# Kernel optimization log

Hardware: AMD Instinct MI355X
Metric: run time of the kernel (lower is better)

The kernel has to match this reference:

```python
import jax, jax.numpy as jnp
import numpy as np

D_IN = 768
D_OUT = 768
NUM_HEADS = 12


def setup_inputs() -> dict:
    key = jax.random.key(0)
    kx, kq, kk, kv, ko = jax.random.split(key, 5)
    x = jax.random.normal(kx, (4, 2048, D_IN), dtype=jnp.float32)
    # torch.rand -> uniform [0,1)
    w_query = jax.random.uniform(kq, (D_IN, D_OUT), dtype=jnp.float32)
    w_key = jax.random.uniform(kk, (D_IN, D_OUT), dtype=jnp.float32)
    w_value = jax.random.uniform(kv, (D_IN, D_OUT), dtype=jnp.float32)
    out_proj = jax.random.uniform(ko, (D_IN, D_OUT), dtype=jnp.float32)
    return {"x": x, "w_query": w_query, "w_key": w_key, "w_value": w_value, "out_proj": out_proj}


def reference(x, w_query, w_key, w_value, out_proj):
    b, n, _ = x.shape
    hd = D_OUT // NUM_HEADS  # head_dim
    q = (x @ w_query).reshape(b, n, NUM_HEADS, hd).transpose(0, 2, 1, 3)  # [b,h,n,hd]
    k = (x @ w_key).reshape(b, n, NUM_HEADS, hd).transpose(0, 2, 1, 3)
    v = (x @ w_value).reshape(b, n, NUM_HEADS, hd).transpose(0, 2, 1, 3)
    scores = jnp.einsum('bhqd,bhkd->bhqk', q, k)
    causal = jnp.triu(jnp.ones((n, n), dtype=bool), k=1)
    scores = jnp.where(causal, -jnp.inf, scores)
    attn = jax.nn.softmax(scores / jnp.sqrt(jnp.float32(hd)), axis=-1)
    # dropout p=0.0 -> identity
    ctx = jnp.einsum('bhqk,bhkd->bhqd', attn, v).transpose(0, 2, 1, 3).reshape(b, n, D_OUT)
    return ctx @ out_proj
```

## Files before the change

### kernel.cpp

```cpp
#include <hip/hip_runtime.h>

typedef __bf16    bf16x8 __attribute__((ext_vector_type(8)));
typedef _Float16  f16x8  __attribute__((ext_vector_type(8)));
typedef _Float16  f16x4  __attribute__((ext_vector_type(4)));
typedef float     f32x4  __attribute__((ext_vector_type(4)));

#define MFMA16(a,b,c)  __builtin_amdgcn_mfma_f32_16x16x32_bf16((a),(b),(c),0,0,0)
#define MFMAF16(a,b,c) __builtin_amdgcn_mfma_f32_16x16x32_f16((a),(b),(c),0,0,0)

#define AS1(p) (const __attribute__((address_space(1))) void*)(p)
#define AS3(p) (__attribute__((address_space(3))) void*)(p)
#define GLL16(g, l) __builtin_amdgcn_global_load_lds(AS1(g), AS3(l), 16, 0, 0)

__device__ __forceinline__ float fexp2(float x) {
  float r; asm("v_exp_f32 %0, %1" : "=v"(r) : "v"(x)); return r;
}

#define QSCALE 0.18033688011112042f

__global__ __launch_bounds__(256) void k_conv_x(const float* __restrict__ x,
                                                __bf16* __restrict__ xh,
                                                __bf16* __restrict__ xl) {
  int i = blockIdx.x * 256 + threadIdx.x;
  const float4* p = (const float4*)x + (size_t)i * 2;
  float4 a = p[0], b = p[1];
  float v[8] = {a.x, a.y, a.z, a.w, b.x, b.y, b.z, b.w};
  bf16x8 h, l;
#pragma unroll
  for (int j = 0; j < 8; ++j) {
    __bf16 hh = (__bf16)v[j];
    h[j] = hh;
    l[j] = (__bf16)(v[j] - (float)hh);
  }
  *(bf16x8*)(xh + (size_t)i * 8) = h;
  *(bf16x8*)(xl + (size_t)i * 8) = l;
}

__global__ __launch_bounds__(256) void k_conv_w(const float* __restrict__ wq,
                                                const float* __restrict__ wk,
                                                const float* __restrict__ wv,
                                                const float* __restrict__ op,
                                                __bf16* __restrict__ wt_h,
                                                __bf16* __restrict__ wt_l,
                                                _Float16* __restrict__ wot) {
  __shared__ float tile[32][33];
  int bid = blockIdx.x;
  int m = bid / 576, rem = bid % 576;
  int tr = rem / 24, tc = rem % 24;
  const float* src = (m == 0) ? wq : (m == 1) ? wk : (m == 2) ? wv : op;
  int tx = threadIdx.x & 31, ty = threadIdx.x >> 5;
  int r0 = tr * 32, c0 = tc * 32;
#pragma unroll
  for (int j = 0; j < 4; ++j)
    tile[ty + j * 8][tx] = src[(size_t)(r0 + ty + j * 8) * 768 + c0 + tx];
  __syncthreads();
#pragma unroll
  for (int j = 0; j < 4; ++j) {
    float v = tile[tx][ty + j * 8];
    size_t o = (size_t)(c0 + ty + j * 8) * 768 + r0 + tx;
    if (m < 3) {
      size_t oo = (size_t)m * (768 * 768) + o;
      __bf16 h = (__bf16)v;
      wt_h[oo] = h;
      wt_l[oo] = (__bf16)(v - (float)h);
    } else {
      wot[o] = (_Float16)v;
    }
  }
}

__global__ __launch_bounds__(256) void k_qk_gemm(
    const __bf16* __restrict__ Ah, const __bf16* __restrict__ Al,
    const __bf16* __restrict__ Bh, const __bf16* __restrict__ Bl,
    _Float16* __restrict__ qf_o, _Float16* __restrict__ kf_o) {
  __shared__ __align__(16) __bf16 AsH[2][128 * 32];
  __shared__ __align__(16) __bf16 AsL[2][128 * 32];
  __shared__ __align__(16) __bf16 BsH[2][128 * 32];
  __shared__ __align__(16) __bf16 BsL[2][128 * 32];
  int t = threadIdx.x, lane = t & 63, wid = t >> 6;
  int l15 = lane & 15, lh = lane >> 4;
  int bid = blockIdx.x;
  int mt = bid & 63, nt = bid >> 6;
  int m0 = mt * 128, n0 = nt * 128;
  int wr = wid >> 1, wc = wid & 1;
  f32x4 acc[4][4];
#pragma unroll
  for (int i = 0; i < 4; ++i)
#pragma unroll
    for (int j = 0; j < 4; ++j) acc[i][j] = (f32x4){0.f, 0.f, 0.f, 0.f};

  int row0 = t >> 2;
  int kkA = (((t & 3) ^ ((row0 >> 1) & 3)) << 3);
  char* lAH[2] = {(char*)AsH[0] + wid * 1024, (char*)AsH[1] + wid * 1024};
  char* lAL[2] = {(char*)AsL[0] + wid * 1024, (char*)AsL[1] + wid * 1024};
  char* lBH[2] = {(char*)BsH[0] + wid * 1024, (char*)BsH[1] + wid * 1024};
  char* lBL[2] = {(char*)BsL[0] + wid * 1024, (char*)BsL[1] + wid * 1024};

#define QK_STAGE(bb, k0s) do {                                               \
    size_t a0 = (size_t)(m0 + row0) * 768 + (k0s) + kkA;                     \
    size_t a1 = a0 + (size_t)64 * 768;                                       \
    size_t b0 = (size_t)(n0 + row0) * 768 + (k0s) + kkA;                     \
    size_t b1 = b0 + (size_t)64 * 768;                                       \
    GLL16(Ah + a0, lAH[bb]); GLL16(Ah + a1, lAH[bb] + 4096);                 \
    GLL16(Bh + b0, lBH[bb]); GLL16(Bh + b1, lBH[bb] + 4096);                 \
    GLL16(Al + a0, lAL[bb]); GLL16(Al + a1, lAL[bb] + 4096);                 \
    GLL16(Bl + b0, lBL[bb]); GLL16(Bl + b1, lBL[bb] + 4096);                 \
  } while (0)

  QK_STAGE(0, 0);
  asm volatile("s_waitcnt vmcnt(0)" ::: "memory");
  __syncthreads();

  for (int tt = 0; tt < 24; ++tt) {
    int cur = tt & 1;
    if (tt < 23) QK_STAGE(cur ^ 1, (tt + 1) * 32);

    bf16x8 af[4], alf[4], bf_[4], blf[4];
#pragma unroll
    for (int i = 0; i < 4; ++i) {
      int rowA = wr * 64 + i * 16 + l15;
      int aoff = rowA * 64 + (((lh ^ (rowA >> 1)) & 3) << 4);
      int rowB = wc * 64 + i * 16 + l15;
      int boff = rowB * 64 + (((lh ^ (rowB >> 1)) & 3) << 4);
      af[i]  = *(const bf16x8*)((char*)AsH[cur] + aoff);
      alf[i] = *(const bf16x8*)((char*)AsL[cur] + aoff);
      bf_[i] = *(const bf16x8*)((char*)BsH[cur] + boff);
      blf[i] = *(const bf16x8*)((char*)BsL[cur] + boff);
    }
    __builtin_amdgcn_s_setprio(1);
#pragma unroll
    for (int i = 0; i < 4; ++i)
#pragma unroll
      for (int j = 0; j < 4; ++j) {
        acc[i][j] = MFMA16(af[i], bf_[j], acc[i][j]);
        acc[i][j] = MFMA16(af[i], blf[j], acc[i][j]);
        acc[i][j] = MFMA16(alf[i], bf_[j], acc[i][j]);
      }
    __builtin_amdgcn_s_setprio(0);
    asm volatile("s_waitcnt vmcnt(0)" ::: "memory");
    __syncthreads();
  }
#undef QK_STAGE

#pragma unroll
  for (int j = 0; j < 4; ++j) {
    int c = n0 + wc * 64 + j * 16 + l15;
    int which = c / 768; int cc = c - which * 768;
    int hh = cc >> 6, d = cc & 63;
#pragma unroll
    for (int i = 0; i < 4; ++i)
#pragma unroll
      for (int r = 0; r < 4; ++r) {
        int m = m0 + wr * 64 + i * 16 + lh * 4 + r;
        int bb = m >> 11, n = m & 2047;
        float v = acc[i][j][r];
        size_t o = ((size_t)(bb * 12 + hh) * 2048 + n) * 64 + d;
        if (which == 0) qf_o[o] = (_Float16)(v * QSCALE);
        else            kf_o[o] = (_Float16)v;
      }
  }
}

__global__ __launch_bounds__(256) void k_v_gemm(
    const __bf16* __restrict__ A, const __bf16* __restrict__ Bt,
    _Float16* __restrict__ vT_o) {
  __shared__ __align__(16) __bf16 As[2][128 * 32];
  __shared__ __align__(16) __bf16 Bs[2][128 * 32];
  int t = threadIdx.x, lane = t & 63, wid = t >> 6;
  int l15 = lane & 15, lh = lane >> 4;
  int bid = blockIdx.x;
  int mt = bid & 63, nt = bid >> 6;
  int m0 = mt * 128, n0 = 1536 + nt * 128;
  int wr = wid >> 1, wc = wid & 1;
  f32x4 acc[4][4];
#pragma unroll
  for (int i = 0; i < 4; ++i)
#pragma unroll
    for (int j = 0; j < 4; ++j) acc[i][j] = (f32x4){0.f, 0.f, 0.f, 0.f};
  int row0 = t >> 2;
  int kkA = (((t & 3) ^ ((row0 >> 1) & 3)) << 3);
  char* lA[2] = {(char*)As[0] + wid * 1024, (char*)As[1] + wid * 1024};
  char* lB[2] = {(char*)Bs[0] + wid * 1024, (char*)Bs[1] + wid * 1024};

#define V_STAGE(bb, k0s) do {                                                \
    size_t a0 = (size_t)(m0 + row0) * 768 + (k0s) + kkA;                     \
    size_t b0 = (size_t)(n0 + row0) * 768 + (k0s) + kkA;                     \
    GLL16(A + a0, lA[bb]);  GLL16(A + a0 + (size_t)64 * 768, lA[bb] + 4096); \
    GLL16(Bt + b0, lB[bb]); GLL16(Bt + b0 + (size_t)64 * 768, lB[bb] + 4096);\
  } while (0)

  V_STAGE(0, 0);
  asm volatile("s_waitcnt vmcnt(0)" ::: "memory");
  __syncthreads();

  for (int tt = 0; tt < 24; ++tt) {
    int cur = tt & 1;
    if (tt < 23) V_STAGE(cur ^ 1, (tt + 1) * 32);
    bf16x8 af[4], bf_[4];
#pragma unroll
    for (int i = 0; i < 4; ++i) {
      int rowA = wr * 64 + i * 16 + l15;
      int aoff = rowA * 64 + (((lh ^ (rowA >> 1)) & 3) << 4);
      int rowB = wc * 64 + i * 16 + l15;
      int boff = rowB * 64 + (((lh ^ (rowB >> 1)) & 3) << 4);
      af[i]  = *(const bf16x8*)((char*)As[cur] + aoff);
      bf_[i] = *(const bf16x8*)((char*)Bs[cur] + boff);
    }
    __builtin_amdgcn_s_setprio(1);
#pragma unroll
    for (int i = 0; i < 4; ++i)
#pragma unroll
      for (int j = 0; j < 4; ++j) acc[i][j] = MFMA16(af[i], bf_[j], acc[i][j]);
    __builtin_amdgcn_s_setprio(0);
    asm volatile("s_waitcnt vmcnt(0)" ::: "memory");
    __syncthreads();
  }
#undef V_STAGE

#pragma unroll
  for (int j = 0; j < 4; ++j) {
    int c = n0 + wc * 64 + j * 16 + l15;
    int cc = c - 1536;
    int hh = cc >> 6, d = cc & 63;
#pragma unroll
    for (int i = 0; i < 4; ++i)
#pragma unroll
      for (int r = 0; r < 4; ++r) {
        int m = m0 + wr * 64 + i * 16 + lh * 4 + r;
        int bb = m >> 11, n = m & 2047;
        vT_o[((size_t)(bb * 12 + hh) * 64 + d) * 2048 + n] = (_Float16)acc[i][j][r];
      }
  }
}

__global__ __launch_bounds__(256) void k_attn(
    const _Float16* __restrict__ Qf, const _Float16* __restrict__ Kf,
    const _Float16* __restrict__ Vt, _Float16* __restrict__ ctx) {
  __shared__ __align__(16) _Float16 Ks[2][64 * 64];
  __shared__ __align__(16) _Float16 Vs[2][64 * 64];
  __shared__ __align__(16) _Float16 Pt[4][32 * 64];
  int t = threadIdx.x, lane = t & 63, wid = t >> 6;
  int l15 = lane & 15, lh = lane >> 4;
  int bid = blockIdx.x;
  int bh = bid % 48;
  int qt = 15 - bid / 48;
  int qbase = qt * 128 + wid * 32;
  size_t base = (size_t)bh * (2048 * 64);
  char* ptw = (char*)Pt[wid];

  int skey = t >> 3, sdb = t & 7;
  int ssw = (sdb ^ (skey & 7)) * 8;
  const _Float16* ksrc = Kf + base + (size_t)skey * 64 + ssw;
  const _Float16* vsrc = Vt + base + (size_t)skey * 2048 + ssw;
  char* dK[2] = {(char*)Ks[0] + wid * 1024, (char*)Ks[1] + wid * 1024};
  char* dV[2] = {(char*)Vs[0] + wid * 1024, (char*)Vs[1] + wid * 1024};

#define ATT_STAGE(bb, k0s) do {                                    \
    GLL16(ksrc + (size_t)(k0s) * 64, dK[bb]);                      \
    GLL16(ksrc + (size_t)(k0s) * 64 + 2048, dK[bb] + 4096);        \
    GLL16(vsrc + (k0s), dV[bb]);                                   \
    GLL16(vsrc + (k0s) + 32 * 2048, dV[bb] + 4096);                \
  } while (0)

  f16x8 qf[2][2];
#pragma unroll
  for (int i = 0; i < 2; ++i)
#pragma unroll
    for (int kk = 0; kk < 2; ++kk)
      qf[i][kk] = *(const f16x8*)(Qf + base +
          (size_t)(qbase + i * 16 + l15) * 64 + kk * 32 + lh * 8);

  f32x4 o[2][4];
#pragma unroll
  for (int i = 0; i < 2; ++i)
#pragma unroll
    for (int d = 0; d < 4; ++d) o[i][d] = (f32x4){0.f, 0.f, 0.f, 0.f};
  float mrun[2] = {-1e30f, -1e30f}, lrun[2] = {0.f, 0.f};

  int nIter = 2 * qt + 2;
  ATT_STAGE(0, 0);
  asm volatile("s_waitcnt vmcnt(0)" ::: "memory");
  __syncthreads();

  for (int it = 0; it < nIter; ++it) {
    int cur = it & 1;
    int k0 = it * 64;
    if (it + 1 < nIter) ATT_STAGE(cur ^ 1, k0 + 64);

    if (k0 <= qbase + 31) {
      f32x4 s[4][2];
#pragma unroll
      for (int j = 0; j < 4; ++j)
#pragma unroll
        for (int i = 0; i < 2; ++i) s[j][i] = (f32x4){0.f, 0.f, 0.f, 0.f};
      __builtin_amdgcn_s_setprio(1);
#pragma unroll
      for (int j = 0; j < 4; ++j) {
        int kr = j * 16 + l15;
#pragma unroll
        for (int kk = 0; kk < 2; ++kk) {
          int sw = ((kk * 4 + lh) ^ (kr & 7)) << 4;
          f16x8 kf = *(const f16x8*)((char*)Ks[cur] + kr * 128 + sw);
          s[j][0] = MFMAF16(kf, qf[0][kk], s[j][0]);
          s[j][1] = MFMAF16(kf, qf[1][kk], s[j][1]);
        }
      }
      __builtin_amdgcn_s_setprio(0);

      if (k0 + 63 > qbase) {
#pragma unroll
        for (int j = 0; j < 4; ++j)
#pragma unroll
          for (int i = 0; i < 2; ++i)
#pragma unroll
            for (int r = 0; r < 4; ++r) {
              int key = k0 + j * 16 + lh * 4 + r;
              int qg = qbase + i * 16 + l15;
              if (key > qg) s[j][i][r] = -1e30f;
            }
      }

#pragma unroll
      for (int i = 0; i < 2; ++i) {
        float m01 = fmaxf(fmaxf(s[0][i][0], s[0][i][1]), fmaxf(s[0][i][2], s[0][i][3]));
        float m23 = fmaxf(fmaxf(s[1][i][0], s[1][i][1]), fmaxf(s[1][i][2], s[1][i][3]));
        float m45 = fmaxf(fmaxf(s[2][i][0], s[2][i][1]), fmaxf(s[2][i][2], s[2][i][3]));
        float m67 = fmaxf(fmaxf(s[3][i][0], s[3][i][1]), fmaxf(s[3][i][2], s[3][i][3]));
        float mx = fmaxf(fmaxf(m01, m23), fmaxf(m45, m67));
        mx = fmaxf(mx, __shfl_xor(mx, 16));
        mx = fmaxf(mx, __shfl_xor(mx, 32));
        float mn = fmaxf(mrun[i], mx);
        float alpha = fexp2(mrun[i] - mn);
        mrun[i] = mn;
        float rsum = 0.f;
#pragma unroll
        for (int j = 0; j < 4; ++j)
#pragma unroll
          for (int r = 0; r < 4; ++r) {
            float e = fexp2(s[j][i][r] - mn);
            s[j][i][r] = e;
            rsum += e;
          }
        rsum += __shfl_xor(rsum, 16);
        rsum += __shfl_xor(rsum, 32);
        lrun[i] = lrun[i] * alpha + rsum;
#pragma unroll
        for (int d = 0; d < 4; ++d) o[i][d] *= alpha;
#pragma unroll
        for (int j = 0; j < 4; ++j) {
          f16x4 pk = { (_Float16)s[j][i][0], (_Float16)s[j][i][1],
                       (_Float16)s[j][i][2], (_Float16)s[j][i][3] };
          int row = 16 * i + l15;
          int boff = (row * 128 + j * 32 + lh * 8) ^ ((l15 & 7) << 4);
          *(f16x4*)(ptw + boff) = pk;
        }
      }
      asm volatile("" ::: "memory");
      f16x8 pa[2][2];
#pragma unroll
      for (int i = 0; i < 2; ++i)
#pragma unroll
        for (int kk = 0; kk < 2; ++kk) {
          int row = 16 * i + l15;
          int boff = (row * 128 + kk * 64 + lh * 16) ^ ((l15 & 7) << 4);
          pa[i][kk] = *(const f16x8*)(ptw + boff);
        }
      asm volatile("" ::: "memory");

      __builtin_amdgcn_s_setprio(1);
#pragma unroll
      for (int dt = 0; dt < 4; ++dt) {
        int dr = dt * 16 + l15;
#pragma unroll
        for (int kk = 0; kk < 2; ++kk) {
          int sw = ((kk * 4 + lh) ^ (dr & 7)) << 4;
          f16x8 vf = *(const f16x8*)((char*)Vs[cur] + dr * 128 + sw);
          o[0][dt] = MFMAF16(vf, pa[0][kk], o[0][dt]);
          o[1][dt] = MFMAF16(vf, pa[1][kk], o[1][dt]);
        }
      }
      __builtin_amdgcn_s_setprio(0);
    }
    asm volatile("s_waitcnt vmcnt(0)" ::: "memory");
    __syncthreads();
  }
#undef ATT_STAGE

  int b = bh / 12, hh = bh - (bh / 12) * 12;
  float inv[2] = {1.f / lrun[0], 1.f / lrun[1]};
#pragma unroll
  for (int i = 0; i < 2; ++i)
#pragma unroll
    for (int dt = 0; dt < 4; ++dt) {
      f16x4 cw = { (_Float16)(o[i][dt][0] * inv[i]), (_Float16)(o[i][dt][1] * inv[i]),
                   (_Float16)(o[i][dt][2] * inv[i]), (_Float16)(o[i][dt][3] * inv[i]) };
      int row = 16 * i + l15;
      int boff = (row * 128 + dt * 32 + lh * 8) ^ ((l15 & 7) << 4);
      *(f16x4*)(ptw + boff) = cw;
    }
  asm volatile("" ::: "memory");
  int lr = lane >> 1, hc = lane & 1;
#pragma unroll
  for (int q16 = 0; q16 < 4; ++q16) {
    int boff = (lr * 128 + hc * 64 + q16 * 16) ^ ((lr & 7) << 4);
    f16x8 vv = *(const f16x8*)(ptw + boff);
    *(f16x8*)(ctx + ((size_t)b * 2048 + qbase + lr) * 768 + hh * 64 + hc * 32 + q16 * 8) = vv;
  }
}

__global__ __launch_bounds__(256) void k_out_gemm(const _Float16* __restrict__ A,
                                                  const _Float16* __restrict__ Bt,
                                                  float* __restrict__ C) {
  __shared__ __align__(16) _Float16 As[2][128 * 32];
  __shared__ __align__(16) _Float16 Bs[2][128 * 32];
  int t = threadIdx.x, lane = t & 63, wid = t >> 6;
  int l15 = lane & 15, lh = lane >> 4;
  int bid = blockIdx.x;
  int mt = bid & 63, nt = bid >> 6;
  int m0 = mt * 128, n0 = nt * 128;
  int wr = wid >> 1, wc = wid & 1;
  f32x4 acc[4][4];
#pragma unroll
  for (int i = 0; i < 4; ++i)
#pragma unroll
    for (int j = 0; j < 4; ++j) acc[i][j] = (f32x4){0.f, 0.f, 0.f, 0.f};
  int row0 = t >> 2;
  int kkA = (((t & 3) ^ ((row0 >> 1) & 3)) << 3);
  char* lA[2] = {(char*)As[0] + wid * 1024, (char*)As[1] + wid * 1024};
  char* lB[2] = {(char*)Bs[0] + wid * 1024, (char*)Bs[1] + wid * 1024};

#define OUT_STAGE(bb, k0s) do {                                              \
    size_t a0 = (size_t)(m0 + row0) * 768 + (k0s) + kkA;                     \
    size_t b0 = (size_t)(n0 + row0) * 768 + (k0s) + kkA;                     \
    GLL16(A + a0, lA[bb]);  GLL16(A + a0 + (size_t)64 * 768, lA[bb] + 4096); \
    GLL16(Bt + b0, lB[bb]); GLL16(Bt + b0 + (size_t)64 * 768, lB[bb] + 4096);\
  } while (0)

  OUT_STAGE(0, 0);
  asm volatile("s_waitcnt vmcnt(0)" ::: "memory");
  __syncthreads();

  for (int tt = 0; tt < 24; ++tt) {
    int cur = tt & 1;
    if (tt < 23) OUT_STAGE(cur ^ 1, (tt + 1) * 32);
    f16x8 af[4], bf_[4];
#pragma unroll
    for (int i = 0; i < 4; ++i) {
      int rowA = wr * 64 + i * 16 + l15;
      int aoff = rowA * 64 + (((lh ^ (rowA >> 1)) & 3) << 4);
      int rowB = wc * 64 + i * 16 + l15;
      int boff = rowB * 64 + (((lh ^ (rowB >> 1)) & 3) << 4);
      af[i]  = *(const f16x8*)((char*)As[cur] + aoff);
      bf_[i] = *(const f16x8*)((char*)Bs[cur] + boff);
    }
    __builtin_amdgcn_s_setprio(1);
#pragma unroll
    for (int i = 0; i < 4; ++i)
#pragma unroll
      for (int j = 0; j < 4; ++j) acc[i][j] = MFMAF16(af[i], bf_[j], acc[i][j]);
    __builtin_amdgcn_s_setprio(0);
    asm volatile("s_waitcnt vmcnt(0)" ::: "memory");
    __syncthreads();
  }
#undef OUT_STAGE

#pragma unroll
  for (int j = 0; j < 4; ++j) {
    int c = n0 + wc * 64 + j * 16 + l15;
#pragma unroll
    for (int i = 0; i < 4; ++i)
#pragma unroll
      for (int r = 0; r < 4; ++r) {
        int m = m0 + wr * 64 + i * 16 + lh * 4 + r;
        C[(size_t)m * 768 + c] = acc[i][j][r];
      }
  }
}

extern "C" void kernel_launch(void* const* d_in, const int* in_sizes, int n_in,
                              void* d_out, int out_size, void* d_ws, size_t ws_size,
                              hipStream_t stream) {
  const float* x  = (const float*)d_in[0];
  const float* wq = (const float*)d_in[1];
  const float* wk = (const float*)d_in[2];
  const float* wv = (const float*)d_in[3];
  const float* op = (const float*)d_in[4];
  float* out = (float*)d_out;

  char* ws = (char*)d_ws;
  const size_t SZ = (size_t)8192 * 768 * 2;
  __bf16* xh     = (__bf16*)ws;    ws += SZ;
  __bf16* xl     = (__bf16*)ws;    ws += SZ;
  __bf16* wt_h   = (__bf16*)ws;    ws += (size_t)2304 * 768 * 2;
  __bf16* wt_l   = (__bf16*)ws;    ws += (size_t)2304 * 768 * 2;
  _Float16* wot  = (_Float16*)ws;  ws += (size_t)768 * 768 * 2;
  _Float16* qf   = (_Float16*)ws;  ws += SZ;
  _Float16* kf   = (_Float16*)ws;  ws += SZ;
  _Float16* vT   = (_Float16*)ws;  ws += SZ;
  _Float16* ctx  = (_Float16*)ws;  ws += SZ;

  hipLaunchKernelGGL(k_conv_x, dim3(3072), dim3(256), 0, stream, x, xh, xl);
  hipLaunchKernelGGL(k_conv_w, dim3(2304), dim3(256), 0, stream,
                     wq, wk, wv, op, wt_h, wt_l, wot);
  hipLaunchKernelGGL(k_qk_gemm, dim3(64 * 12), dim3(256), 0, stream,
                     xh, xl, wt_h, wt_l, qf, kf);
  hipLaunchKernelGGL(k_v_gemm, dim3(64 * 6), dim3(256), 0, stream, xh, wt_h, vT);
  hipLaunchKernelGGL(k_attn, dim3(48 * 16), dim3(256), 0, stream, qf, kf, vT, ctx);
  hipLaunchKernelGGL(k_out_gemm, dim3(64 * 6), dim3(256), 0, stream, ctx, wot, out);
}
```

Measured before the change: 246.6 us.

## Triple-buffer GEMM LDS stages with partial vmcnt waits and lazy softmax rescale

Moves the three projection GEMMs from double to triple buffering in shared memory. Each iteration prefetches two stages ahead and waits with vmcnt(4) instead of draining every load before the barrier, so global-to-LDS copies overlap more of the MFMA work. In the QK GEMM only the hi parts get three buffers and the lo parts stay double-buffered with one-ahead loads. Separately, the flash-attention loop now skips the running-max update and the rescale of the output and sum when the new max stays within a threshold of the old one. This trades extra LDS use, and possibly occupancy, plus a wider fp16 range in the P values for fewer waits and fewer exp and multiply operations.

```diff
diff --git a/kernel.cpp b/kernel.cpp
--- a/kernel.cpp
+++ b/kernel.cpp
@@ -11,6 +11,10 @@
 #define AS1(p) (const __attribute__((address_space(1))) void*)(p)
 #define AS3(p) (__attribute__((address_space(3))) void*)(p)
 #define GLL16(g, l) __builtin_amdgcn_global_load_lds(AS1(g), AS3(l), 16, 0, 0)
+
+#define VMCNT4 asm volatile("s_waitcnt vmcnt(4)" ::: "memory")
+#define VMCNT0 asm volatile("s_waitcnt vmcnt(0)" ::: "memory")
+#define RBAR   do { __builtin_amdgcn_s_barrier(); asm volatile("" ::: "memory"); } while (0)
 
 __device__ __forceinline__ float fexp2(float x) {
   float r; asm("v_exp_f32 %0, %1" : "=v"(r) : "v"(x)); return r;
@@ -73,9 +77,9 @@
     const __bf16* __restrict__ Ah, const __bf16* __restrict__ Al,
     const __bf16* __restrict__ Bh, const __bf16* __restrict__ Bl,
     _Float16* __restrict__ qf_o, _Float16* __restrict__ kf_o) {
-  __shared__ __align__(16) __bf16 AsH[2][128 * 32];
+  __shared__ __align__(16) __bf16 AsH[3][128 * 32];
+  __shared__ __align__(16) __bf16 BsH[3][128 * 32];
   __shared__ __align__(16) __bf16 AsL[2][128 * 32];
-  __shared__ __align__(16) __bf16 BsH[2][128 * 32];
   __shared__ __align__(16) __bf16 BsL[2][128 * 32];
   int t = threadIdx.x, lane = t & 63, wid = t >> 6;
   int l15 = lane & 15, lh = lane >> 4;
@@ -91,29 +95,36 @@
 
   int row0 = t >> 2;
   int kkA = (((t & 3) ^ ((row0 >> 1) & 3)) << 3);
-  char* lAH[2] = {(char*)AsH[0] + wid * 1024, (char*)AsH[1] + wid * 1024};
-  char* lAL[2] = {(char*)AsL[0] + wid * 1024, (char*)AsL[1] + wid * 1024};
-  char* lBH[2] = {(char*)BsH[0] + wid * 1024, (char*)BsH[1] + wid * 1024};
-  char* lBL[2] = {(char*)BsL[0] + wid * 1024, (char*)BsL[1] + wid * 1024};
-
-#define QK_STAGE(bb, k0s) do {                                               \
-    size_t a0 = (size_t)(m0 + row0) * 768 + (k0s) + kkA;                     \
-    size_t a1 = a0 + (size_t)64 * 768;                                       \
-    size_t b0 = (size_t)(n0 + row0) * 768 + (k0s) + kkA;                     \
-    size_t b1 = b0 + (size_t)64 * 768;                                       \
-    GLL16(Ah + a0, lAH[bb]); GLL16(Ah + a1, lAH[bb] + 4096);                 \
-    GLL16(Bh + b0, lBH[bb]); GLL16(Bh + b1, lBH[bb] + 4096);                 \
-    GLL16(Al + a0, lAL[bb]); GLL16(Al + a1, lAL[bb] + 4096);                 \
-    GLL16(Bl + b0, lBL[bb]); GLL16(Bl + b1, lBL[bb] + 4096);                 \
+  const __bf16* gAh = Ah + (size_t)(m0 + row0) * 768 + kkA;
+  const __bf16* gAl = Al + (size_t)(m0 + row0) * 768 + kkA;
+  const __bf16* gBh = Bh + (size_t)(n0 + row0) * 768 + kkA;
+  const __bf16* gBl = Bl + (size_t)(n0 + row0) * 768 + kkA;
+  const size_t RSK = (size_t)64 * 768;
+
+#define STG_HI(b, k0s) do {                                                  \
+    char* dA = (char*)AsH[b] + wid * 1024;                                   \
+    char* dB = (char*)BsH[b] + wid * 1024;                                   \
+    GLL16(gAh + (k0s), dA); GLL16(gAh + (k0s) + RSK, dA + 4096);             \
+    GLL16(gBh + (k0s), dB); GLL16(gBh + (k0s) + RSK, dB + 4096);             \
   } while (0)
-
-  QK_STAGE(0, 0);
-  asm volatile("s_waitcnt vmcnt(0)" ::: "memory");
-  __syncthreads();
-
+#define STG_LO(b, k0s) do {                                                  \
+    char* dA = (char*)AsL[b] + wid * 1024;                                   \
+    char* dB = (char*)BsL[b] + wid * 1024;                                   \
+    GLL16(gAl + (k0s), dA); GLL16(gAl + (k0s) + RSK, dA + 4096);             \
+    GLL16(gBl + (k0s), dB); GLL16(gBl + (k0s) + RSK, dB + 4096);             \
+  } while (0)
+
+  STG_HI(0, 0);
+  STG_LO(0, 0);
+  STG_HI(1, 32);
+  VMCNT4;
+  RBAR;
+
+  int cur3 = 0, curl = 0;
   for (int tt = 0; tt < 24; ++tt) {
-    int cur = tt & 1;
-    if (tt < 23) QK_STAGE(cur ^ 1, (tt + 1) * 32);
+    if (tt < 23) STG_LO(curl ^ 1, (tt + 1) * 32);
+    int tg3 = cur3 + 2; if (tg3 >= 3) tg3 -= 3;
+    if (tt < 22) STG_HI(tg3, (tt + 2) * 32);
 
     bf16x8 af[4], alf[4], bf_[4], blf[4];
 #pragma unroll
@@ -122,10 +133,10 @@
       int aoff = rowA * 64 + (((lh ^ (rowA >> 1)) & 3) << 4);
       int rowB = wc * 64 + i * 16 + l15;
       int boff = rowB * 64 + (((lh ^ (rowB >> 1)) & 3) << 4);
-      af[i]  = *(const bf16x8*)((char*)AsH[cur] + aoff);
-      alf[i] = *(const bf16x8*)((char*)AsL[cur] + aoff);
-      bf_[i] = *(const bf16x8*)((char*)BsH[cur] + boff);
-      blf[i] = *(const bf16x8*)((char*)BsL[cur] + boff);
+      af[i]  = *(const bf16x8*)((char*)AsH[cur3] + aoff);
+      alf[i] = *(const bf16x8*)((char*)AsL[curl] + aoff);
+      bf_[i] = *(const bf16x8*)((char*)BsH[cur3] + boff);
+      blf[i] = *(const bf16x8*)((char*)BsL[curl] + boff);
     }
     __builtin_amdgcn_s_setprio(1);
 #pragma unroll
@@ -137,10 +148,14 @@
         acc[i][j] = MFMA16(alf[i], bf_[j], acc[i][j]);
       }
     __builtin_amdgcn_s_setprio(0);
-    asm volatile("s_waitcnt vmcnt(0)" ::: "memory");
-    __syncthreads();
-  }
-#undef QK_STAGE
+
+    if (tt < 22) { VMCNT4; } else { VMCNT0; }
+    RBAR;
+    cur3 = cur3 + 1 == 3 ? 0 : cur3 + 1;
+    curl ^= 1;
+  }
+#undef STG_HI
+#undef STG_LO
 
 #pragma unroll
   for (int j = 0; j < 4; ++j) {
@@ -164,8 +179,8 @@
 __global__ __launch_bounds__(256) void k_v_gemm(
     const __bf16* __restrict__ A, const __bf16* __restrict__ Bt,
     _Float16* __restrict__ vT_o) {
-  __shared__ __align__(16) __bf16 As[2][128 * 32];
-  __shared__ __align__(16) __bf16 Bs[2][128 * 32];
+  __shared__ __align__(16) __bf16 As[3][128 * 32];
+  __shared__ __align__(16) __bf16 Bs[3][128 * 32];
   int t = threadIdx.x, lane = t & 63, wid = t >> 6;
   int l15 = lane & 15, lh = lane >> 4;
   int bid = blockIdx.x;
@@ -179,23 +194,26 @@
     for (int j = 0; j < 4; ++j) acc[i][j] = (f32x4){0.f, 0.f, 0.f, 0.f};
   int row0 = t >> 2;
   int kkA = (((t & 3) ^ ((row0 >> 1) & 3)) << 3);
-  char* lA[2] = {(char*)As[0] + wid * 1024, (char*)As[1] + wid * 1024};
-  char* lB[2] = {(char*)Bs[0] + wid * 1024, (char*)Bs[1] + wid * 1024};
-
-#define V_STAGE(bb, k0s) do {                                                \
-    size_t a0 = (size_t)(m0 + row0) * 768 + (k0s) + kkA;                     \
-    size_t b0 = (size_t)(n0 + row0) * 768 + (k0s) + kkA;                     \
-    GLL16(A + a0, lA[bb]);  GLL16(A + a0 + (size_t)64 * 768, lA[bb] + 4096); \
-    GLL16(Bt + b0, lB[bb]); GLL16(Bt + b0 + (size_t)64 * 768, lB[bb] + 4096);\
+  const __bf16* gA = A + (size_t)(m0 + row0) * 768 + kkA;
+  const __bf16* gB = Bt + (size_t)(n0 + row0) * 768 + kkA;
+  const size_t RSK = (size_t)64 * 768;
+
+#define STG(b, k0s) do {                                                     \
+    char* dA = (char*)As[b] + wid * 1024;                                    \
+    char* dB = (char*)Bs[b] + wid * 1024;                                    \
+    GLL16(gA + (k0s), dA); GLL16(gA + (k0s) + RSK, dA + 4096);               \
+    GLL16(gB + (k0s), dB); GLL16(gB + (k0s) + RSK, dB + 4096);               \
   } while (0)
 
-  V_STAGE(0, 0);
-  asm volatile("s_waitcnt vmcnt(0)" ::: "memory");
-  __syncthreads();
-
+  STG(0, 0);
+  STG(1, 32);
+  VMCNT4;
+  RBAR;
+
+  int cur3 = 0;
   for (int tt = 0; tt < 24; ++tt) {
-    int cur = tt & 1;
-    if (tt < 23) V_STAGE(cur ^ 1, (tt + 1) * 32);
+    int tg3 = cur3 + 2; if (tg3 >= 3) tg3 -= 3;
+    if (tt < 22) STG(tg3, (tt + 2) * 32);
     bf16x8 af[4], bf_[4];
 #pragma unroll
     for (int i = 0; i < 4; ++i) {
@@ -203,8 +221,8 @@
       int aoff = rowA * 64 + (((lh ^ (rowA >> 1)) & 3) << 4);
       int rowB = wc * 64 + i * 16 + l15;
       int boff = rowB * 64 + (((lh ^ (rowB >> 1)) & 3) << 4);
-      af[i]  = *(const bf16x8*)((char*)As[cur] + aoff);
-      bf_[i] = *(const bf16x8*)((char*)Bs[cur] + boff);
+      af[i]  = *(const bf16x8*)((char*)As[cur3] + aoff);
+      bf_[i] = *(const bf16x8*)((char*)Bs[cur3] + boff);
     }
     __builtin_amdgcn_s_setprio(1);
 #pragma unroll
@@ -212,10 +230,11 @@
 #pragma unroll
       for (int j = 0; j < 4; ++j) acc[i][j] = MFMA16(af[i], bf_[j], acc[i][j]);
     __builtin_amdgcn_s_setprio(0);
-    asm volatile("s_waitcnt vmcnt(0)" ::: "memory");
-    __syncthreads();
-  }
-#undef V_STAGE
+    if (tt < 22) { VMCNT4; } else { VMCNT0; }
+    RBAR;
+    cur3 = cur3 + 1 == 3 ? 0 : cur3 + 1;
+  }
+#undef STG
 
 #pragma unroll
   for (int j = 0; j < 4; ++j) {
@@ -329,9 +348,16 @@
         float mx = fmaxf(fmaxf(m01, m23), fmaxf(m45, m67));
         mx = fmaxf(mx, __shfl_xor(mx, 16));
         mx = fmaxf(mx, __shfl_xor(mx, 32));
-        float mn = fmaxf(mrun[i], mx);
-        float alpha = fexp2(mrun[i] - mn);
-        mrun[i] = mn;
+        bool keep = !__all(mx <= mrun[i] + 8.f);
+        float mn = mrun[i];
+        if (keep) {
+          mn = fmaxf(mrun[i], mx);
+          float alpha = fexp2(mrun[i] - mn);
+          mrun[i] = mn;
+          lrun[i] *= alpha;
+#pragma unroll
+          for (int d = 0; d < 4; ++d) o[i][d] *= alpha;
+        }
         float rsum = 0.f;
 #pragma unroll
         for (int j = 0; j < 4; ++j)
@@ -343,9 +369,7 @@
           }
         rsum += __shfl_xor(rsum, 16);
         rsum += __shfl_xor(rsum, 32);
-        lrun[i] = lrun[i] * alpha + rsum;
-#pragma unroll
-        for (int d = 0; d < 4; ++d) o[i][d] *= alpha;
+        lrun[i] += rsum;
 #pragma unroll
         for (int j = 0; j < 4; ++j) {
           f16x4 pk = { (_Float16)s[j][i][0], (_Float16)s[j][i][1],
@@ -411,8 +435,8 @@
 __global__ __launch_bounds__(256) void k_out_gemm(const _Float16* __restrict__ A,
                                                   const _Float16* __restrict__ Bt,
                                                   float* __restrict__ C) {
-  __shared__ __align__(16) _Float16 As[2][128 * 32];
-  __shared__ __align__(16) _Float16 Bs[2][128 * 32];
+  __shared__ __align__(16) _Float16 As[3][128 * 32];
+  __shared__ __align__(16) _Float16 Bs[3][128 * 32];
   int t = threadIdx.x, lane = t & 63, wid = t >> 6;
   int l15 = lane & 15, lh = lane >> 4;
   int bid = blockIdx.x;
@@ -426,23 +450,26 @@
     for (int j = 0; j < 4; ++j) acc[i][j] = (f32x4){0.f, 0.f, 0.f, 0.f};
   int row0 = t >> 2;
   int kkA = (((t & 3) ^ ((row0 >> 1) & 3)) << 3);
-  char* lA[2] = {(char*)As[0] + wid * 1024, (char*)As[1] + wid * 1024};
-  char* lB[2] = {(char*)Bs[0] + wid * 1024, (char*)Bs[1] + wid * 1024};
-
-#define OUT_STAGE(bb, k0s) do {                                              \
-    size_t a0 = (size_t)(m0 + row0) * 768 + (k0s) + kkA;                     \
-    size_t b0 = (size_t)(n0 + row0) * 768 + (k0s) + kkA;                     \
-    GLL16(A + a0, lA[bb]);  GLL16(A + a0 + (size_t)64 * 768, lA[bb] + 4096); \
-    GLL16(Bt + b0, lB[bb]); GLL16(Bt + b0 + (size_t)64 * 768, lB[bb] + 4096);\
+  const _Float16* gA = A + (size_t)(m0 + row0) * 768 + kkA;
+  const _Float16* gB = Bt + (size_t)(n0 + row0) * 768 + kkA;
+  const size_t RSK = (size_t)64 * 768;
+
+#define STG(b, k0s) do {                                                     \
+    char* dA = (char*)As[b] + wid * 1024;                                    \
+    char* dB = (char*)Bs[b] + wid * 1024;                                    \
+    GLL16(gA + (k0s), dA); GLL16(gA + (k0s) + RSK, dA + 4096);               \
+    GLL16(gB + (k0s), dB); GLL16(gB + (k0s) + RSK, dB + 4096);               \
   } while (0)
 
-  OUT_STAGE(0, 0);
-  asm volatile("s_waitcnt vmcnt(0)" ::: "memory");
-  __syncthreads();
-
+  STG(0, 0);
+  STG(1, 32);
+  VMCNT4;
+  RBAR;
+
+  int cur3 = 0;
   for (int tt = 0; tt < 24; ++tt) {
-    int cur = tt & 1;
-    if (tt < 23) OUT_STAGE(cur ^ 1, (tt + 1) * 32);
+    int tg3 = cur3 + 2; if (tg3 >= 3) tg3 -= 3;
+    if (tt < 22) STG(tg3, (tt + 2) * 32);
     f16x8 af[4], bf_[4];
 #pragma unroll
     for (int i = 0; i < 4; ++i) {
@@ -450,8 +477,8 @@
       int aoff = rowA * 64 + (((lh ^ (rowA >> 1)) & 3) << 4);
       int rowB = wc * 64 + i * 16 + l15;
       int boff = rowB * 64 + (((lh ^ (rowB >> 1)) & 3) << 4);
-      af[i]  = *(const f16x8*)((char*)As[cur] + aoff);
-      bf_[i] = *(const f16x8*)((char*)Bs[cur] + boff);
+      af[i]  = *(const f16x8*)((char*)As[cur3] + aoff);
+      bf_[i] = *(const f16x8*)((char*)Bs[cur3] + boff);
     }
     __builtin_amdgcn_s_setprio(1);
 #pragma unroll
@@ -459,10 +486,11 @@
 #pragma unroll
       for (int j = 0; j < 4; ++j) acc[i][j] = MFMAF16(af[i], bf_[j], acc[i][j]);
     __builtin_amdgcn_s_setprio(0);
-    asm volatile("s_waitcnt vmcnt(0)" ::: "memory");
-    __syncthreads();
-  }
-#undef OUT_STAGE
+    if (tt < 22) { VMCNT4; } else { VMCNT0; }
+    RBAR;
+    cur3 = cur3 + 1 == 3 ? 0 : cur3 + 1;
+  }
+#undef STG
 
 #pragma unroll
   for (int j = 0; j < 4; ++j) {
```

After: 264.8 us. 7.4% more time.
